# Kernel optimization log

Hardware: AMD Instinct MI355X
Metric: run time of the kernel (lower is better)

The kernel has to match this reference:

```python
import jax, jax.numpy as jnp
import numpy as np
from itertools import combinations, product

NQ = 10
DIM = 2 ** NQ
DEPTH = 1
ENC_PAIRS = [(q, q + 1) for q in range(0, NQ - 1, 2)] + [(q, q + 1) for q in range(1, NQ - 1, 2)]  # brick layer: even then odd
PYR = [(i, i + 1) for layer in range(NQ - 1) for i in range(NQ - layer - 1)]  # pyramid RBS wire pairs (45)
OBS_PAIRS = list(combinations(range(NQ), 2))  # 45 pairwise 2-local observables

_P = {'I': np.eye(2, dtype=np.complex128),
      'X': np.array([[0, 1], [1, 0]], dtype=np.complex128),
      'Y': np.array([[0, -1j], [1j, 0]], dtype=np.complex128),
      'Z': np.array([[1, 0], [0, -1]], dtype=np.complex128)}
_WORDS = [''.join(w) for w in product('IXYZ', repeat=2)][1:]  # PennyLane pauli_basis order, identity excluded
P15 = jnp.asarray(np.stack([np.kron(_P[w[0]], _P[w[1]]) for w in _WORDS]).astype(np.complex64))
XXm = jnp.asarray(np.kron(_P['X'], _P['X']).astype(np.complex64))
YYm = jnp.asarray(np.kron(_P['Y'], _P['Y']).astype(np.complex64))
ZZm = jnp.asarray(np.kron(_P['Z'], _P['Z']).astype(np.complex64))
I4 = jnp.eye(4, dtype=jnp.complex64)
_TRIL_I, _TRIL_J = np.tril_indices(4, -1)  # order matches create_Hermitian's count+j indexing


def _u3(t, p, l):
    c = jnp.cos(t / 2).astype(jnp.complex64)
    s = jnp.sin(t / 2).astype(jnp.complex64)
    return jnp.stack([jnp.stack([c, -jnp.exp(1j * l) * s]),
                      jnp.stack([jnp.exp(1j * p) * s, jnp.exp(1j * (p + l)) * c])])


def _ising(phi, P):
    # exp(-i*phi/2 * P) for P in {XX, YY, ZZ} (P^2 = I)
    return jnp.cos(phi / 2) * I4 - 1j * jnp.sin(phi / 2) * P


def _apply1(psi, U, w):
    # psi: (B, 2, ..., 2); single-qubit gate U (2,2) on wire w
    psi = jnp.moveaxis(psi, 1 + w, -1)
    sh = psi.shape
    out = jnp.einsum('ij,brj->bri', U, psi.reshape(sh[0], -1, 2)).reshape(sh)
    return jnp.moveaxis(out, -1, 1 + w)


def _apply2(psi, U, a, b):
    # two-qubit gate on wires (a,b), a is most-significant (PennyLane wire order). U: (4,4) or batched (B,4,4)
    psi = jnp.moveaxis(psi, (1 + a, 1 + b), (-2, -1))
    sh = psi.shape
    flat = psi.reshape(sh[0], -1, 4)
    eq = 'bij,brj->bri' if U.ndim == 3 else 'ij,brj->bri'
    out = jnp.einsum(eq, U, flat).reshape(sh)
    return jnp.moveaxis(out, (-2, -1), (1 + a, 1 + b))


def _build_H(A, B, D):
    # create_Hermitian: lower triangle A+iB, diag[0:3] = D[1:4], diag[3]=0, then h + h^dagger
    n = A.shape[0]
    h = jnp.zeros((n, 4, 4), jnp.complex64)
    h = h.at[:, _TRIL_I, _TRIL_J].set(A.astype(jnp.complex64) + 1j * B.astype(jnp.complex64))
    d = np.arange(3)
    h = h.at[:, d, d].set(D[:, 1:4].astype(jnp.complex64))
    return h + jnp.conj(jnp.swapaxes(h, -1, -2))


def setup_inputs() -> dict:
    key = jax.random.key(0)
    ks = jax.random.split(key, 9)
    f32 = jnp.float32
    return {
        'x': jax.random.normal(ks[0], (256, 512), f32),
        'W1': jax.random.normal(ks[1], (512, 256), f32) * (512 ** -0.5),
        'b1': jnp.zeros((256,), f32),
        'W2': jax.random.normal(ks[2], (256, 135), f32) * (256 ** -0.5),
        'b2': jnp.zeros((135,), f32),
        'qvit_params': 0.01 * jax.random.normal(ks[3], (DEPTH, len(PYR), 12), f32),
        'A': 2.0 * jax.random.normal(ks[4], (len(OBS_PAIRS), 6), f32),
        'B': 2.0 * jax.random.normal(ks[5], (len(OBS_PAIRS), 6), f32),
        'D': 2.0 * jax.random.normal(ks[6], (len(OBS_PAIRS), 4), f32),
    }


def reference(x, W1, b1, W2, b2, qvit_params, A, B, D):
    Bsz = x.shape[0]
    # enc_proj: Linear -> SiLU -> Linear
    enc = jax.nn.silu(x @ W1 + b1) @ W2 + b2  # (B, 135)
    # Brick-layer SpecialUnitary encoding: U = exp(i * sum theta_m P_m) via eigh
    theta = enc.reshape(Bsz, len(ENC_PAIRS), 15).astype(jnp.complex64)
    Hg = jnp.einsum('bgm,mij->bgij', theta, P15)  # Hermitian generators (B, 9, 4, 4)
    ew, V = jnp.linalg.eigh(Hg)
    Ue = jnp.einsum('bgik,bgk,bgjk->bgij', V, jnp.exp(1j * ew.astype(jnp.complex64)), jnp.conj(V))
    # |0...0>
    psi = jnp.zeros((Bsz, DIM), jnp.complex64).at[:, 0].set(1.0).reshape((Bsz,) + (2,) * NQ)
    for g, (a, b) in enumerate(ENC_PAIRS):
        psi = _apply2(psi, Ue[:, g], a, b)
    # QViT pyramid ansatz
    for ly in range(DEPTH):
        for g, (a, b) in enumerate(PYR):
            p = qvit_params[ly, g]
            psi = _apply1(psi, _u3(p[0], p[1], p[2]), a)
            psi = _apply2(psi, _ising(p[3], XXm), a, b)
            psi = _apply2(psi, _ising(p[4], YYm), a, b)
            psi = _apply2(psi, _ising(p[5], ZZm), a, b)
            psi = _apply1(psi, _u3(p[6], p[7], p[8]), a)
            psi = _apply2(psi, _ising(p[9], XXm), a, b)
            psi = _apply2(psi, _ising(p[10], YYm), a, b)
            psi = _apply2(psi, _ising(p[11], ZZm), a, b)
    # Pairwise ANO Hermitian expectations
    Hobs = _build_H(A, B, D)  # (45, 4, 4)
    outs = []
    for w, (a, b) in enumerate(OBS_PAIRS):
        pm = jnp.moveaxis(psi, (1 + a, 1 + b), (1, 2)).reshape(Bsz, 4, -1)
        outs.append(jnp.real(jnp.einsum('bir,ij,bjr->b', jnp.conj(pm), Hobs[w], pm)))
    return jnp.stack(outs, axis=1).astype(jnp.float32)
```

## Files before the change

kernel.cpp:

```cpp
#include <hip/hip_runtime.h>
#include <math.h>

#define NOBS 45
typedef float2 c32;

constexpr int OAc[NOBS] = {
    0,0,0,0,0,0,0,0,0, 1,1,1,1,1,1,1,1, 2,2,2,2,2,2,2, 3,3,3,3,3,3,
    4,4,4,4,4, 5,5,5,5, 6,6,6, 7,7, 8};
constexpr int OBc[NOBS] = {
    1,2,3,4,5,6,7,8,9, 2,3,4,5,6,7,8,9, 3,4,5,6,7,8,9, 4,5,6,7,8,9,
    5,6,7,8,9, 6,7,8,9, 7,8,9, 8,9, 9};

__device__ __forceinline__ c32 cfma(c32 a, c32 b, c32 c) {
    c.x = fmaf(a.x, b.x, fmaf(-a.y, b.y, c.x));
    c.y = fmaf(a.x, b.y, fmaf(a.y, b.x, c.y));
    return c;
}
__device__ __forceinline__ c32 cmul(c32 a, c32 b) {
    return make_float2(a.x * b.x - a.y * b.y, a.x * b.y + a.y * b.x);
}

template <int CTRL>
__device__ __forceinline__ float dppf(float x) {
    return __uint_as_float((unsigned)__builtin_amdgcn_update_dpp(
        0, (int)__float_as_uint(x), CTRL, 0xF, 0xF, true));
}
__device__ __forceinline__ float swap32f(float a) {
    auto r = __builtin_amdgcn_permlane32_swap(__float_as_uint(a), __float_as_uint(a), false, false);
    return (__uint_as_float(r[0]) + __uint_as_float(r[1])) - a;
}
#if __has_builtin(__builtin_amdgcn_permlane16_swap)
__device__ __forceinline__ float swap16f(float a) {
    auto r = __builtin_amdgcn_permlane16_swap(__float_as_uint(a), __float_as_uint(a), false, false);
    return (__uint_as_float(r[0]) + __uint_as_float(r[1])) - a;
}
#else
__device__ __forceinline__ float swap16f(float a) { return __shfl_xor(a, 16, 64); }
#endif
__device__ __forceinline__ float swz4f(float a) {
    return __uint_as_float(__builtin_amdgcn_ds_swizzle(__float_as_uint(a), 0x101F));
}
template <int M>
__device__ __forceinline__ float exf(float x) {
    float r = x;
    if constexpr ((M & 3) == 1) r = dppf<0xB1>(r);
    else if constexpr ((M & 3) == 2) r = dppf<0x4E>(r);
    else if constexpr ((M & 3) == 3) r = dppf<0x1B>(r);
    if constexpr (M & 4)  r = swz4f(r);
    if constexpr (M & 8)  r = dppf<0x128>(r);
    if constexpr (M & 16) r = swap16f(r);
    if constexpr (M & 32) r = swap32f(r);
    return r;
}
template <int M>
__device__ __forceinline__ c32 exch(c32 a) { return make_float2(exf<M>(a.x), exf<M>(a.y)); }

__device__ __forceinline__ float wave_reduce63(float x) {
    x += dppf<0x111>(x);
    x += dppf<0x112>(x);
    x += dppf<0x114>(x);
    x += dppf<0x118>(x);
    x += dppf<0x142>(x);
    x += dppf<0x143>(x);
    return x;
}

__device__ __forceinline__ int insert2(int t, int pl, int ph) {
    int low  = t & ((1 << pl) - 1);
    int rest = t >> pl;
    int nm   = ph - 1 - pl;
    int mid  = rest & ((1 << nm) - 1);
    int high = rest >> nm;
    return low | (mid << (pl + 1)) | (high << (ph + 1));
}

template <int W>
__device__ __forceinline__ c32 pE(int r, int c) {
    if constexpr (W == 0) return make_float2((r == c) ? 1.f : 0.f, 0.f);
    else if constexpr (W == 1) return make_float2((r != c) ? 1.f : 0.f, 0.f);
    else if constexpr (W == 2) return make_float2(0.f, (r == c) ? 0.f : ((r == 0) ? -1.f : 1.f));
    else return make_float2((r == c) ? ((r == 0) ? 1.f : -1.f) : 0.f, 0.f);
}
template <int W0, int W1>
__device__ __forceinline__ void paccum(c32& H, float th, int i1, int i2, int j1, int j2) {
    c32 a = pE<W0>(i1, j1), b = pE<W1>(i2, j2);
    c32 p = cmul(a, b);
    H.x = fmaf(th, p.x, H.x);
    H.y = fmaf(th, p.y, H.y);
}

struct F8v { c32 u[8]; };
struct FLoc { c32 a[4]; c32 b[4]; };
struct F4 { c32 uS, uB, uA, uC; };

__device__ __forceinline__ F8v loadF8(const c32* __restrict__ U, int rr) {
    F8v f;
    const c32* R = U + (rr << 3);
#pragma unroll
    for (int i = 0; i < 8; i++) f.u[i] = R[i];
    return f;
}
template <int LB>
__device__ __forceinline__ FLoc loadLocLane(const c32* __restrict__ U, int ln) {
    int lb = (ln >> LB) & 1;
    const c32* R0 = U + lb * 4;
    const c32* R1 = U + (2 | lb) * 4;
    FLoc f;
    f.a[0] = R0[lb]; f.a[1] = R0[lb ^ 1]; f.a[2] = R0[2 | lb]; f.a[3] = R0[2 | (lb ^ 1)];
    f.b[0] = R1[lb]; f.b[1] = R1[lb ^ 1]; f.b[2] = R1[2 | lb]; f.b[3] = R1[2 | (lb ^ 1)];
    return f;
}
template <int LB>
__device__ __forceinline__ void applyLocLane(c32 v[2], const FLoc& f) {
    c32 p0 = exch<(1 << LB)>(v[0]);
    c32 p1 = exch<(1 << LB)>(v[1]);
    c32 n0 = cfma(f.a[3], p1, cfma(f.a[2], v[1], cfma(f.a[1], p0, cmul(f.a[0], v[0]))));
    c32 n1 = cfma(f.b[3], p1, cfma(f.b[2], v[1], cfma(f.b[1], p0, cmul(f.b[0], v[0]))));
    v[0] = n0; v[1] = n1;
}
template <int QA, int QB>
__device__ __forceinline__ F4 loadL2(const c32* __restrict__ U, int ln) {
    int bA = (ln >> QA) & 1, bB = (ln >> QB) & 1;
    int r = (bA << 1) | bB;
    const c32* Ur = U + r * 4;
    F4 f;
    f.uS = Ur[r]; f.uB = Ur[r ^ 1]; f.uA = Ur[r ^ 2]; f.uC = Ur[r ^ 3];
    return f;
}
template <int QA, int QB>
__device__ __forceinline__ void applyL2(c32 v[2], const F4& f) {
    c32 pB[2], pA[2], pC[2];
#pragma unroll
    for (int lc = 0; lc < 2; lc++) pB[lc] = exch<(1 << QB)>(v[lc]);
#pragma unroll
    for (int lc = 0; lc < 2; lc++) pA[lc] = exch<(1 << QA)>(v[lc]);
#pragma unroll
    for (int lc = 0; lc < 2; lc++) pC[lc] = exch<(1 << QA)>(pB[lc]);
#pragma unroll
    for (int lc = 0; lc < 2; lc++)
        v[lc] = cfma(f.uC, pC[lc], cfma(f.uA, pA[lc], cfma(f.uB, pB[lc], cmul(f.uS, v[lc]))));
}

__device__ __forceinline__ void dumpV2(const c32 v[2], c32* __restrict__ psi, int t) {
    psi[t * 2] = v[0]; psi[t * 2 + 1] = v[1];
}
__device__ __forceinline__ void loadV2(c32 v[2], const c32* __restrict__ psi, int t) {
    v[0] = psi[t * 2]; v[1] = psi[t * 2 + 1];
}
template <int PA, int PB>
__device__ __forceinline__ void ldsApply2(const F8v& f, const c32* __restrict__ src,
                                          c32* __restrict__ dst, int g, int rr) {
    int base = insert2(g, PA, PB);
    constexpr int oa = 1 << PA, ob = 1 << PB;
    c32 g0 = src[base], g1 = src[base + ob], g2 = src[base + oa], g3 = src[base + oa + ob];
    c32 n0 = cfma(f.u[3], g3, cfma(f.u[2], g2, cfma(f.u[1], g1, cmul(f.u[0], g0))));
    c32 n1 = cfma(f.u[7], g3, cfma(f.u[6], g2, cfma(f.u[5], g1, cmul(f.u[4], g0))));
    dst[base + rr * oa] = n0;
    dst[base + rr * oa + ob] = n1;
}

__global__ __launch_bounds__(512, 1) void mega_kernel(
    const float* __restrict__ x,  const float* __restrict__ W1, const float* __restrict__ b1,
    const float* __restrict__ W2, const float* __restrict__ b2, const float* __restrict__ qp,
    const float* __restrict__ Am, const float* __restrict__ Bm, const float* __restrict__ Dm,
    float* __restrict__ out) {
    __shared__ __align__(16) c32 psiS[2048];
    __shared__ c32 UeS[144];
    __shared__ c32 GpS[720];
    __shared__ float HbS[720];
    __shared__ float encS0[136], encS1[136];
    __shared__ float redS[NOBS * 8];

    const int b = blockIdx.x, t = threadIdx.x, ln = t & 63;
    const int gg = t & 255, rr = t >> 8, wv = t >> 6;
    float* F = (float*)psiS;
    c32* psiA = psiS;
    c32* psiB = psiS + 1024;

    if (t < 128) ((float4*)F)[t] = ((const float4*)(x + (size_t)b * 512))[t];
    __syncthreads();
    {
        int q = t & 63, sl = t >> 6;
        float4 a4 = make_float4(0.f, 0.f, 0.f, 0.f);
#pragma unroll 16
        for (int kk = 0; kk < 64; kk++) {
            int k = sl * 64 + kk;
            float xk = F[k];
            const float4 w = *(const float4*)(W1 + (size_t)k * 256 + q * 4);
            a4.x = fmaf(xk, w.x, a4.x); a4.y = fmaf(xk, w.y, a4.y);
            a4.z = fmaf(xk, w.z, a4.z); a4.w = fmaf(xk, w.w, a4.w);
        }
        *(float4*)(F + 512 + sl * 256 + q * 4) = a4;
    }
    __syncthreads();
    if (t < 256) {
        float hv = b1[t];
#pragma unroll
        for (int s = 0; s < 8; s++) hv += F[512 + s * 256 + t];
        hv = hv / (1.f + __expf(-hv));
        F[2560 + t] = hv;
    }
    __syncthreads();
    if (t < 135) {
        float a0 = b2[t], a1 = 0.f;
#pragma unroll 16
        for (int k = 0; k < 64; k++) {
            a0 = fmaf(F[2560 + k],      W2[(size_t)k * 135 + t],        a0);
            a1 = fmaf(F[2560 + 64 + k], W2[(size_t)(64 + k) * 135 + t], a1);
        }
        encS0[t] = a0 + a1;
    } else if (t >= 256 && t < 391) {
        int c = t - 256;
        float a0 = 0.f, a1 = 0.f;
#pragma unroll 16
        for (int k = 0; k < 64; k++) {
            a0 = fmaf(F[2560 + 128 + k], W2[(size_t)(128 + k) * 135 + c], a0);
            a1 = fmaf(F[2560 + 192 + k], W2[(size_t)(192 + k) * 135 + c], a1);
        }
        encS1[c] = a0 + a1;
    }
    __syncthreads();

    c32* Mm = psiS;
    c32* Rb = psiS + 144;
    c32* TA = psiS + 288;
    if (t < 144) {
        int m = t >> 4, e = t & 15, i = e >> 2, j = e & 3;
        int i1 = i >> 1, i2 = i & 1, j1 = j >> 1, j2 = j & 1;
        const int o = m * 15;
        c32 H = make_float2(0.f, 0.f);
#define TH(J) (encS0[o + (J)] + encS1[o + (J)])
        paccum<0,1>(H, TH(0),  i1,i2,j1,j2); paccum<0,2>(H, TH(1),  i1,i2,j1,j2);
        paccum<0,3>(H, TH(2),  i1,i2,j1,j2); paccum<1,0>(H, TH(3),  i1,i2,j1,j2);
        paccum<1,1>(H, TH(4),  i1,i2,j1,j2); paccum<1,2>(H, TH(5),  i1,i2,j1,j2);
        paccum<1,3>(H, TH(6),  i1,i2,j1,j2); paccum<2,0>(H, TH(7),  i1,i2,j1,j2);
        paccum<2,1>(H, TH(8),  i1,i2,j1,j2); paccum<2,2>(H, TH(9),  i1,i2,j1,j2);
        paccum<2,3>(H, TH(10), i1,i2,j1,j2); paccum<3,0>(H, TH(11), i1,i2,j1,j2);
        paccum<3,1>(H, TH(12), i1,i2,j1,j2); paccum<3,2>(H, TH(13), i1,i2,j1,j2);
        paccum<3,3>(H, TH(14), i1,i2,j1,j2);
#undef TH
        const float sc = 1.f / 64.f;
        Mm[t] = make_float2(-H.y * sc, H.x * sc);
        Rb[t] = make_float2((i == j) ? 1.f : 0.f, 0.f);
    } else if (t >= 384 && t < 384 + NOBS) {
        const int w = t - 384;
        float* Hf = HbS + w * 16;
        Hf[0] = 2.f * Dm[w * 4 + 1];
        Hf[1] = 2.f * Dm[w * 4 + 2];
        Hf[2] = 2.f * Dm[w * 4 + 3];
        Hf[3] = 0.f;
#pragma unroll
        for (int k = 0; k < 6; k++) {
            Hf[4 + 2 * k] = 2.f * Am[w * 6 + k];
            Hf[5 + 2 * k] = 2.f * Bm[w * 6 + k];
        }
    }
    __syncthreads();
    c32 Mrow[4];
    if (t < 144) {
        int m = t >> 4, i = (t & 15) >> 2;
#pragma unroll
        for (int k = 0; k < 4; k++) Mrow[k] = Mm[m * 16 + i * 4 + k];
    }
#pragma unroll 1
    for (int step = 0; step < 13; step++) {
        if (t < 144) {
            int m = t >> 4, e = t & 15, i = e >> 2, j = e & 3;
            const c32* cur = (step & 1) ? UeS : Rb;
            c32 acc = make_float2(0.f, 0.f);
            c32 outv;
            if (step < 7) {
#pragma unroll
                for (int k = 0; k < 4; k++) acc = cfma(Mrow[k], cur[m * 16 + k * 4 + j], acc);
                float inv = 1.f / (float)(7 - step);
                outv = make_float2(fmaf(acc.x, inv, (i == j) ? 1.f : 0.f), acc.y * inv);
            } else {
#pragma unroll
                for (int k = 0; k < 4; k++)
                    acc = cfma(cur[m * 16 + i * 4 + k], cur[m * 16 + k * 4 + j], acc);
                outv = acc;
            }
            ((step & 1) ? Rb : UeS)[t] = outv;
        } else if (t >= 144 && t < 234 && step < 8) {
            int pt = t - 144, g = pt >> 1, ih = (pt & 1) << 1;
            const float* p = qp + g * 12;
            const c32* src = ((step & 1) ? TA : GpS) + g * 16;
            c32* dst = ((step & 1) ? GpS : TA) + g * 16;
#pragma unroll
            for (int r2 = 0; r2 < 2; r2++) {
                int i = ih + r2, i1 = i >> 1, i2 = i & 1;
                c32 rowv[4];
                if (step == 0) {
                    float s, c; __sincosf(p[0] * 0.5f, &s, &c);
                    c32 u0, u1;
                    if (i1 == 0) { u0 = make_float2(c, 0.f);
                                   u1 = make_float2(-__cosf(p[2]) * s, -__sinf(p[2]) * s); }
                    else { u0 = make_float2(__cosf(p[1]) * s, __sinf(p[1]) * s);
                           u1 = make_float2(__cosf(p[1] + p[2]) * c, __sinf(p[1] + p[2]) * c); }
#pragma unroll
                    for (int jj = 0; jj < 4; jj++) rowv[jj] = make_float2(0.f, 0.f);
                    rowv[i2] = u0; rowv[2 | i2] = u1;
                } else {
                    c32 coef0, coef1; int c0, c1;
                    if (step == 1 || step == 5) {
                        float s, c; __sincosf(p[step == 1 ? 3 : 9] * 0.5f, &s, &c);
                        c0 = i; coef0 = make_float2(c, 0.f);
                        c1 = i ^ 3; coef1 = make_float2(0.f, -s);
                    } else if (step == 2 || step == 6) {
                        float s, c; __sincosf(p[step == 2 ? 4 : 10] * 0.5f, &s, &c);
                        float yy = (i == 0 || i == 3) ? 1.f : -1.f;
                        c0 = i; coef0 = make_float2(c, 0.f);
                        c1 = i ^ 3; coef1 = make_float2(0.f, s * yy);
                    } else if (step == 3 || step == 7) {
                        float s, c; __sincosf(p[step == 3 ? 5 : 11] * 0.5f, &s, &c);
                        float zz = (i == 0 || i == 3) ? 1.f : -1.f;
                        c0 = i; coef0 = make_float2(c, -s * zz);
                        c1 = i; coef1 = make_float2(0.f, 0.f);
                    } else {
                        float s, c; __sincosf(p[6] * 0.5f, &s, &c);
                        if (i1 == 0) { coef0 = make_float2(c, 0.f);
                                       coef1 = make_float2(-__cosf(p[8]) * s, -__sinf(p[8]) * s); }
                        else { coef0 = make_float2(__cosf(p[7]) * s, __sinf(p[7]) * s);
                               coef1 = make_float2(__cosf(p[7] + p[8]) * c, __sinf(p[7] + p[8]) * c); }
                        c0 = i2; c1 = 2 | i2;
                    }
#pragma unroll
                    for (int jj = 0; jj < 4; jj++)
                        rowv[jj] = cfma(coef0, src[c0 * 4 + jj], cmul(coef1, src[c1 * 4 + jj]));
                }
#pragma unroll
                for (int jj = 0; jj < 4; jj++) dst[i * 4 + jj] = rowv[jj];
            }
        }
        __syncthreads();
    }

    c32 v[2];
    v[0] = make_float2(0.f, 0.f);
    v[1] = make_float2(0.f, 0.f);
    if (t == 0) v[0] = make_float2(1.f, 0.f);

    applyLocLane<0>(v, loadLocLane<0>(UeS + 0, ln));
    applyL2<1, 2>(v, loadL2<1, 2>(UeS + 16, ln));
    applyL2<3, 4>(v, loadL2<3, 4>(UeS + 32, ln));
    applyL2<0, 1>(v, loadL2<0, 1>(UeS + 80, ln));
    applyL2<2, 3>(v, loadL2<2, 3>(UeS + 96, ln));
    dumpV2(v, psiA, t); __syncthreads();
    ldsApply2<6, 7>(loadF8(UeS + 48, rr), psiA, psiB, gg, rr); __syncthreads();
    ldsApply2<8, 9>(loadF8(UeS + 64, rr), psiB, psiA, gg, rr); __syncthreads();
    loadV2(v, psiA, t);
    applyL2<4, 5>(v, loadL2<4, 5>(UeS + 112, ln));
    dumpV2(v, psiA, t); __syncthreads();
    ldsApply2<7, 8>(loadF8(UeS + 128, rr), psiA, psiB, gg, rr); __syncthreads();
    loadV2(v, psiB, t);

    {
        int g = 0;
#pragma unroll
        for (int layer = 0; layer < 9; layer++) {
            const int amax = 8 - layer;
            applyLocLane<0>(v, loadLocLane<0>(GpS + (g++) * 16, ln));
            if (amax >= 1) applyL2<0, 1>(v, loadL2<0, 1>(GpS + (g++) * 16, ln));
            if (amax >= 2) applyL2<1, 2>(v, loadL2<1, 2>(GpS + (g++) * 16, ln));
            if (amax >= 3) applyL2<2, 3>(v, loadL2<2, 3>(GpS + (g++) * 16, ln));
            if (amax >= 4) applyL2<3, 4>(v, loadL2<3, 4>(GpS + (g++) * 16, ln));
            if (amax >= 5) applyL2<4, 5>(v, loadL2<4, 5>(GpS + (g++) * 16, ln));
            if (amax >= 6) {
                dumpV2(v, psiA, t); __syncthreads();
                ldsApply2<6, 7>(loadF8(GpS + (g++) * 16, rr), psiA, psiB, gg, rr);
                __syncthreads();
                if (amax >= 7) {
                    ldsApply2<7, 8>(loadF8(GpS + (g++) * 16, rr), psiB, psiA, gg, rr);
                    __syncthreads();
                    if (amax >= 8) {
                        ldsApply2<8, 9>(loadF8(GpS + (g++) * 16, rr), psiA, psiB, gg, rr);
                        __syncthreads();
                        loadV2(v, psiB, t);
                    } else {
                        loadV2(v, psiA, t);
                    }
                } else {
                    loadV2(v, psiB, t);
                }
            }
        }
    }

    dumpV2(v, psiA, t);
    __syncthreads();
#pragma unroll
    for (int w0 = 0; w0 < NOBS; w0 += 5) {
        float pr[5];
#pragma unroll
        for (int u = 0; u < 5; u++) {
            const int w = w0 + u;
            const int pa = OAc[w], pb = OBc[w];
            const int oa = 1 << pa, ob = 1 << pb;
            int i0 = insert2(gg, pa, pb);
            const float* Hf = HbS + w * 16;
            c32 g0 = psiA[i0], g1 = psiA[i0 + ob], g2 = psiA[i0 + oa], g3 = psiA[i0 + oa + ob];
            float r;
            if (rr == 0) {
                r = Hf[0] * fmaf(g0.x, g0.x, g0.y * g0.y)
                  + Hf[1] * fmaf(g1.x, g1.x, g1.y * g1.y)
                  + Hf[2] * fmaf(g2.x, g2.x, g2.y * g2.y);
                float cx0 = fmaf(g1.x, g0.x, g1.y * g0.y);
                float cy0 = fmaf(g1.x, g0.y, -g1.y * g0.x);
                r = fmaf(Hf[4], cx0, r); r = fmaf(-Hf[5], cy0, r);
                float cx1 = fmaf(g2.x, g0.x, g2.y * g0.y);
                float cy1 = fmaf(g2.x, g0.y, -g2.y * g0.x);
                r = fmaf(Hf[6], cx1, r); r = fmaf(-Hf[7], cy1, r);
            } else {
                float cx0 = fmaf(g2.x, g1.x, g2.y * g1.y);
                float cy0 = fmaf(g2.x, g1.y, -g2.y * g1.x);
                r = Hf[8] * cx0 - Hf[9] * cy0;
                float cx1 = fmaf(g3.x, g0.x, g3.y * g0.y);
                float cy1 = fmaf(g3.x, g0.y, -g3.y * g0.x);
                r = fmaf(Hf[10], cx1, r); r = fmaf(-Hf[11], cy1, r);
                float cx2 = fmaf(g3.x, g1.x, g3.y * g1.y);
                float cy2 = fmaf(g3.x, g1.y, -g3.y * g1.x);
                r = fmaf(Hf[12], cx2, r); r = fmaf(-Hf[13], cy2, r);
                float cx3 = fmaf(g3.x, g2.x, g3.y * g2.y);
                float cy3 = fmaf(g3.x, g2.y, -g3.y * g2.x);
                r = fmaf(Hf[14], cx3, r); r = fmaf(-Hf[15], cy3, r);
            }
            pr[u] = wave_reduce63(r);
        }
        if (ln == 63) {
#pragma unroll
            for (int u = 0; u < 5; u++) redS[(w0 + u) * 8 + wv] = pr[u];
        }
    }
    __syncthreads();
    if (t < NOBS) {
        float s = 0.f;
#pragma unroll
        for (int k = 0; k < 8; k++) s += redS[t * 8 + k];
        out[(size_t)b * NOBS + t] = s;
    }
}

extern "C" void kernel_launch(void* const* d_in, const int* in_sizes, int n_in,
                              void* d_out, int out_size, void* d_ws, size_t ws_size,
                              hipStream_t stream) {
    (void)in_sizes; (void)n_in; (void)out_size; (void)d_ws; (void)ws_size;
    const float* x  = (const float*)d_in[0];
    const float* W1 = (const float*)d_in[1];
    const float* b1 = (const float*)d_in[2];
    const float* W2 = (const float*)d_in[3];
    const float* b2 = (const float*)d_in[4];
    const float* qp = (const float*)d_in[5];
    const float* Am = (const float*)d_in[6];
    const float* Bm = (const float*)d_in[7];
    const float* Dm = (const float*)d_in[8];
    float* out = (float*)d_out;

    hipLaunchKernelGGL(mega_kernel, dim3(256), dim3(512), 0, stream,
                       x, W1, b1, W2, b2, qp, Am, Bm, Dm, out);
}
```

Before: 105.6 us.

## Remap wire-to-slot layout and batch gate coefficient loads ahead of apply

Introduces a wire-to-storage-bit permutation that moves wire 3 to a high slot and wires 4-6 down, so more gates act on register/lane-local bits and the LDS-based two-qubit steps use different bit pairs. Gate coefficient loads for each pyramid layer and for the encoder are hoisted before a scheduling barrier, and the observable phase batches LDS amplitude reads before the arithmetic. This is meant to hide LDS load latency and reduce expensive cross-lane or LDS gate passes, at the cost of higher register pressure and a more intricate index mapping.

```diff
diff --git a/kernel.cpp b/kernel.cpp
--- a/kernel.cpp
+++ b/kernel.cpp
@@ -4,12 +4,15 @@
 #define NOBS 45
 typedef float2 c32;
 
+constexpr int W2S[10] = {0, 1, 2, 4, 5, 6, 3, 7, 8, 9};
 constexpr int OAc[NOBS] = {
     0,0,0,0,0,0,0,0,0, 1,1,1,1,1,1,1,1, 2,2,2,2,2,2,2, 3,3,3,3,3,3,
     4,4,4,4,4, 5,5,5,5, 6,6,6, 7,7, 8};
 constexpr int OBc[NOBS] = {
     1,2,3,4,5,6,7,8,9, 2,3,4,5,6,7,8,9, 3,4,5,6,7,8,9, 4,5,6,7,8,9,
     5,6,7,8,9, 6,7,8,9, 7,8,9, 8,9, 9};
+
+#define SCHED_FENCE() __builtin_amdgcn_sched_barrier(0)
 
 __device__ __forceinline__ c32 cfma(c32 a, c32 b, c32 c) {
     c.x = fmaf(a.x, b.x, fmaf(-a.y, b.y, c.x));
@@ -340,41 +343,64 @@
     v[1] = make_float2(0.f, 0.f);
     if (t == 0) v[0] = make_float2(1.f, 0.f);
 
-    applyLocLane<0>(v, loadLocLane<0>(UeS + 0, ln));
-    applyL2<1, 2>(v, loadL2<1, 2>(UeS + 16, ln));
-    applyL2<3, 4>(v, loadL2<3, 4>(UeS + 32, ln));
-    applyL2<0, 1>(v, loadL2<0, 1>(UeS + 80, ln));
-    applyL2<2, 3>(v, loadL2<2, 3>(UeS + 96, ln));
-    dumpV2(v, psiA, t); __syncthreads();
-    ldsApply2<6, 7>(loadF8(UeS + 48, rr), psiA, psiB, gg, rr); __syncthreads();
-    ldsApply2<8, 9>(loadF8(UeS + 64, rr), psiB, psiA, gg, rr); __syncthreads();
-    loadV2(v, psiA, t);
-    applyL2<4, 5>(v, loadL2<4, 5>(UeS + 112, ln));
-    dumpV2(v, psiA, t); __syncthreads();
-    ldsApply2<7, 8>(loadF8(UeS + 128, rr), psiA, psiB, gg, rr); __syncthreads();
-    loadV2(v, psiB, t);
+    {
+        FLoc e0 = loadLocLane<0>(UeS + 0, ln);
+        F4 e1 = loadL2<1, 3>(UeS + 16, ln);
+        F4 e2 = loadL2<4, 5>(UeS + 32, ln);
+        F4 e3 = loadL2<0, 1>(UeS + 80, ln);
+        F4 e4 = loadL2<3, 4>(UeS + 96, ln);
+        F8v e5 = loadF8(UeS + 48, rr);
+        F8v e6 = loadF8(UeS + 64, rr);
+        SCHED_FENCE();
+        applyLocLane<0>(v, e0);
+        applyL2<1, 3>(v, e1);
+        applyL2<4, 5>(v, e2);
+        applyL2<0, 1>(v, e3);
+        applyL2<3, 4>(v, e4);
+        dumpV2(v, psiA, t); __syncthreads();
+        ldsApply2<3, 7>(e5, psiA, psiB, gg, rr); __syncthreads();
+        ldsApply2<8, 9>(e6, psiB, psiA, gg, rr); __syncthreads();
+        loadV2(v, psiA, t);
+        F4 e7 = loadL2<5, 2>(UeS + 112, ln);
+        F8v e8 = loadF8(UeS + 128, rr);
+        SCHED_FENCE();
+        applyL2<5, 2>(v, e7);
+        dumpV2(v, psiA, t); __syncthreads();
+        ldsApply2<7, 8>(e8, psiA, psiB, gg, rr); __syncthreads();
+        loadV2(v, psiB, t);
+    }
 
     {
         int g = 0;
 #pragma unroll
         for (int layer = 0; layer < 9; layer++) {
             const int amax = 8 - layer;
-            applyLocLane<0>(v, loadLocLane<0>(GpS + (g++) * 16, ln));
-            if (amax >= 1) applyL2<0, 1>(v, loadL2<0, 1>(GpS + (g++) * 16, ln));
-            if (amax >= 2) applyL2<1, 2>(v, loadL2<1, 2>(GpS + (g++) * 16, ln));
-            if (amax >= 3) applyL2<2, 3>(v, loadL2<2, 3>(GpS + (g++) * 16, ln));
-            if (amax >= 4) applyL2<3, 4>(v, loadL2<3, 4>(GpS + (g++) * 16, ln));
-            if (amax >= 5) applyL2<4, 5>(v, loadL2<4, 5>(GpS + (g++) * 16, ln));
+            FLoc h0 = loadLocLane<0>(GpS + g * 16, ln);
+            F4 h1, h2, h3, h4, h5;
+            F8v q1, q2, q3;
+            int gi = g + 1;
+            if (amax >= 1) h1 = loadL2<0, 1>(GpS + (gi++) * 16, ln);
+            if (amax >= 2) h2 = loadL2<1, 3>(GpS + (gi++) * 16, ln);
+            if (amax >= 3) h3 = loadL2<3, 4>(GpS + (gi++) * 16, ln);
+            if (amax >= 4) h4 = loadL2<4, 5>(GpS + (gi++) * 16, ln);
+            if (amax >= 5) h5 = loadL2<5, 2>(GpS + (gi++) * 16, ln);
+            if (amax >= 6) q1 = loadF8(GpS + (gi++) * 16, rr);
+            if (amax >= 7) q2 = loadF8(GpS + (gi++) * 16, rr);
+            if (amax >= 8) q3 = loadF8(GpS + (gi++) * 16, rr);
+            SCHED_FENCE();
+            applyLocLane<0>(v, h0);
+            if (amax >= 1) applyL2<0, 1>(v, h1);
+            if (amax >= 2) applyL2<1, 3>(v, h2);
+            if (amax >= 3) applyL2<3, 4>(v, h3);
+            if (amax >= 4) applyL2<4, 5>(v, h4);
+            if (amax >= 5) applyL2<5, 2>(v, h5);
             if (amax >= 6) {
                 dumpV2(v, psiA, t); __syncthreads();
-                ldsApply2<6, 7>(loadF8(GpS + (g++) * 16, rr), psiA, psiB, gg, rr);
-                __syncthreads();
+                ldsApply2<3, 7>(q1, psiA, psiB, gg, rr); __syncthreads();
                 if (amax >= 7) {
-                    ldsApply2<7, 8>(loadF8(GpS + (g++) * 16, rr), psiB, psiA, gg, rr);
-                    __syncthreads();
+                    ldsApply2<7, 8>(q2, psiB, psiA, gg, rr); __syncthreads();
                     if (amax >= 8) {
-                        ldsApply2<8, 9>(loadF8(GpS + (g++) * 16, rr), psiA, psiB, gg, rr);
-                        __syncthreads();
+                        ldsApply2<8, 9>(q3, psiA, psiB, gg, rr); __syncthreads();
                         loadV2(v, psiB, t);
                     } else {
                         loadV2(v, psiA, t);
@@ -383,6 +409,7 @@
                     loadV2(v, psiB, t);
                 }
             }
+            g = gi;
         }
     }
 
@@ -390,15 +417,24 @@
     __syncthreads();
 #pragma unroll
     for (int w0 = 0; w0 < NOBS; w0 += 5) {
-        float pr[5];
+        c32 vg[5][4];
 #pragma unroll
         for (int u = 0; u < 5; u++) {
             const int w = w0 + u;
-            const int pa = OAc[w], pb = OBc[w];
+            const int pa = W2S[OAc[w]], pb = W2S[OBc[w]];
+            const int pl = (pa < pb) ? pa : pb, ph = (pa < pb) ? pb : pa;
             const int oa = 1 << pa, ob = 1 << pb;
-            int i0 = insert2(gg, pa, pb);
+            int i0 = insert2(gg, pl, ph);
+            vg[u][0] = psiA[i0];      vg[u][1] = psiA[i0 + ob];
+            vg[u][2] = psiA[i0 + oa]; vg[u][3] = psiA[i0 + oa + ob];
+        }
+        SCHED_FENCE();
+        float pr[5];
+#pragma unroll
+        for (int u = 0; u < 5; u++) {
+            const int w = w0 + u;
             const float* Hf = HbS + w * 16;
-            c32 g0 = psiA[i0], g1 = psiA[i0 + ob], g2 = psiA[i0 + oa], g3 = psiA[i0 + oa + ob];
+            c32 g0 = vg[u][0], g1 = vg[u][1], g2 = vg[u][2], g3 = vg[u][3];
             float r;
             if (rr == 0) {
                 r = Hf[0] * fmaf(g0.x, g0.x, g0.y * g0.y)
```

After: 107.6 us. About the same (+2.0%).

## Use 1024 threads with one amplitude per thread and remap qubits to lanes

Applied to the files above, without the earlier changes.

Doubles the block to 1024 threads so each thread holds a single state amplitude instead of two. Qubits are permuted so more gates act on lane bits through cross-lane exchanges, and the rest use LDS passes with one output per thread. Gate coefficients are loaded up front behind a scheduling barrier so LDS reads can overlap. The MLP and observable stages are split across the larger thread count. The cost is more threads per block and possibly higher register pressure under the new launch bounds.

```diff
diff --git a/kernel.cpp b/kernel.cpp
--- a/kernel.cpp
+++ b/kernel.cpp
@@ -4,12 +4,15 @@
 #define NOBS 45
 typedef float2 c32;
 
+constexpr int W2S[10] = {0, 1, 3, 4, 5, 2, 6, 7, 8, 9};
 constexpr int OAc[NOBS] = {
     0,0,0,0,0,0,0,0,0, 1,1,1,1,1,1,1,1, 2,2,2,2,2,2,2, 3,3,3,3,3,3,
     4,4,4,4,4, 5,5,5,5, 6,6,6, 7,7, 8};
 constexpr int OBc[NOBS] = {
     1,2,3,4,5,6,7,8,9, 2,3,4,5,6,7,8,9, 3,4,5,6,7,8,9, 4,5,6,7,8,9,
     5,6,7,8,9, 6,7,8,9, 7,8,9, 8,9, 9};
+
+#define SCHED_FENCE() __builtin_amdgcn_sched_barrier(0)
 
 __device__ __forceinline__ c32 cfma(c32 a, c32 b, c32 c) {
     c.x = fmaf(a.x, b.x, fmaf(-a.y, b.y, c.x));
@@ -89,35 +92,9 @@
     H.y = fmaf(th, p.y, H.y);
 }
 
-struct F8v { c32 u[8]; };
-struct FLoc { c32 a[4]; c32 b[4]; };
 struct F4 { c32 uS, uB, uA, uC; };
-
-__device__ __forceinline__ F8v loadF8(const c32* __restrict__ U, int rr) {
-    F8v f;
-    const c32* R = U + (rr << 3);
-#pragma unroll
-    for (int i = 0; i < 8; i++) f.u[i] = R[i];
-    return f;
-}
-template <int LB>
-__device__ __forceinline__ FLoc loadLocLane(const c32* __restrict__ U, int ln) {
-    int lb = (ln >> LB) & 1;
-    const c32* R0 = U + lb * 4;
-    const c32* R1 = U + (2 | lb) * 4;
-    FLoc f;
-    f.a[0] = R0[lb]; f.a[1] = R0[lb ^ 1]; f.a[2] = R0[2 | lb]; f.a[3] = R0[2 | (lb ^ 1)];
-    f.b[0] = R1[lb]; f.b[1] = R1[lb ^ 1]; f.b[2] = R1[2 | lb]; f.b[3] = R1[2 | (lb ^ 1)];
-    return f;
-}
-template <int LB>
-__device__ __forceinline__ void applyLocLane(c32 v[2], const FLoc& f) {
-    c32 p0 = exch<(1 << LB)>(v[0]);
-    c32 p1 = exch<(1 << LB)>(v[1]);
-    c32 n0 = cfma(f.a[3], p1, cfma(f.a[2], v[1], cfma(f.a[1], p0, cmul(f.a[0], v[0]))));
-    c32 n1 = cfma(f.b[3], p1, cfma(f.b[2], v[1], cfma(f.b[1], p0, cmul(f.b[0], v[0]))));
-    v[0] = n0; v[1] = n1;
-}
+struct F4row { c32 u[4]; };
+
 template <int QA, int QB>
 __device__ __forceinline__ F4 loadL2(const c32* __restrict__ U, int ln) {
     int bA = (ln >> QA) & 1, bB = (ln >> QB) & 1;
@@ -128,38 +105,32 @@
     return f;
 }
 template <int QA, int QB>
-__device__ __forceinline__ void applyL2(c32 v[2], const F4& f) {
-    c32 pB[2], pA[2], pC[2];
-#pragma unroll
-    for (int lc = 0; lc < 2; lc++) pB[lc] = exch<(1 << QB)>(v[lc]);
-#pragma unroll
-    for (int lc = 0; lc < 2; lc++) pA[lc] = exch<(1 << QA)>(v[lc]);
-#pragma unroll
-    for (int lc = 0; lc < 2; lc++) pC[lc] = exch<(1 << QA)>(pB[lc]);
-#pragma unroll
-    for (int lc = 0; lc < 2; lc++)
-        v[lc] = cfma(f.uC, pC[lc], cfma(f.uA, pA[lc], cfma(f.uB, pB[lc], cmul(f.uS, v[lc]))));
-}
-
-__device__ __forceinline__ void dumpV2(const c32 v[2], c32* __restrict__ psi, int t) {
-    psi[t * 2] = v[0]; psi[t * 2 + 1] = v[1];
-}
-__device__ __forceinline__ void loadV2(c32 v[2], const c32* __restrict__ psi, int t) {
-    v[0] = psi[t * 2]; v[1] = psi[t * 2 + 1];
+__device__ __forceinline__ void applyL2(c32& v, const F4& f) {
+    c32 pB = exch<(1 << QB)>(v);
+    c32 pA = exch<(1 << QA)>(v);
+    c32 pC = exch<(1 << QA)>(pB);
+    v = cfma(f.uC, pC, cfma(f.uA, pA, cfma(f.uB, pB, cmul(f.uS, v))));
+}
+
+__device__ __forceinline__ F4row loadF4row(const c32* __restrict__ U, int rr) {
+    F4row f;
+    const c32* R = U + (rr << 2);
+#pragma unroll
+    for (int i = 0; i < 4; i++) f.u[i] = R[i];
+    return f;
 }
 template <int PA, int PB>
-__device__ __forceinline__ void ldsApply2(const F8v& f, const c32* __restrict__ src,
+__device__ __forceinline__ void ldsApply1(const F4row& f, const c32* __restrict__ src,
                                           c32* __restrict__ dst, int g, int rr) {
-    int base = insert2(g, PA, PB);
+    constexpr int PL = (PA < PB) ? PA : PB, PH = (PA < PB) ? PB : PA;
+    int base = insert2(g, PL, PH);
     constexpr int oa = 1 << PA, ob = 1 << PB;
     c32 g0 = src[base], g1 = src[base + ob], g2 = src[base + oa], g3 = src[base + oa + ob];
-    c32 n0 = cfma(f.u[3], g3, cfma(f.u[2], g2, cfma(f.u[1], g1, cmul(f.u[0], g0))));
-    c32 n1 = cfma(f.u[7], g3, cfma(f.u[6], g2, cfma(f.u[5], g1, cmul(f.u[4], g0))));
-    dst[base + rr * oa] = n0;
-    dst[base + rr * oa + ob] = n1;
-}
-
-__global__ __launch_bounds__(512, 1) void mega_kernel(
+    c32 n = cfma(f.u[3], g3, cfma(f.u[2], g2, cfma(f.u[1], g1, cmul(f.u[0], g0))));
+    dst[base + (rr >> 1) * oa + (rr & 1) * ob] = n;
+}
+
+__global__ __launch_bounds__(1024, 4) void mega_kernel(
     const float* __restrict__ x,  const float* __restrict__ W1, const float* __restrict__ b1,
     const float* __restrict__ W2, const float* __restrict__ b2, const float* __restrict__ qp,
     const float* __restrict__ Am, const float* __restrict__ Bm, const float* __restrict__ Dm,
@@ -168,56 +139,48 @@
     __shared__ c32 UeS[144];
     __shared__ c32 GpS[720];
     __shared__ float HbS[720];
-    __shared__ float encS0[136], encS1[136];
-    __shared__ float redS[NOBS * 8];
+    __shared__ float encS[4][136];
+    __shared__ float redS[NOBS * 16];
 
     const int b = blockIdx.x, t = threadIdx.x, ln = t & 63;
-    const int gg = t & 255, rr = t >> 8, wv = t >> 6;
+    const int g4 = t >> 2, rr4 = t & 3, wv = t >> 6;
     float* F = (float*)psiS;
     c32* psiA = psiS;
     c32* psiB = psiS + 1024;
 
-    if (t < 128) ((float4*)F)[t] = ((const float4*)(x + (size_t)b * 512))[t];
-    __syncthreads();
     {
-        int q = t & 63, sl = t >> 6;
+        const int q = t & 63, sl = t >> 6;
+        const float* xrow = x + (size_t)b * 512 + sl * 32;
         float4 a4 = make_float4(0.f, 0.f, 0.f, 0.f);
-#pragma unroll 16
-        for (int kk = 0; kk < 64; kk++) {
-            int k = sl * 64 + kk;
-            float xk = F[k];
-            const float4 w = *(const float4*)(W1 + (size_t)k * 256 + q * 4);
+#pragma unroll 8
+        for (int kk = 0; kk < 32; kk++) {
+            float xk = xrow[kk];
+            const float4 w = *(const float4*)(W1 + (size_t)(sl * 32 + kk) * 256 + q * 4);
             a4.x = fmaf(xk, w.x, a4.x); a4.y = fmaf(xk, w.y, a4.y);
             a4.z = fmaf(xk, w.z, a4.z); a4.w = fmaf(xk, w.w, a4.w);
         }
-        *(float4*)(F + 512 + sl * 256 + q * 4) = a4;
+        *(float4*)(F + sl * 256 + q * 4) = a4;
     }
     __syncthreads();
     if (t < 256) {
         float hv = b1[t];
 #pragma unroll
-        for (int s = 0; s < 8; s++) hv += F[512 + s * 256 + t];
+        for (int s = 0; s < 16; s++) hv += F[s * 256 + t];
         hv = hv / (1.f + __expf(-hv));
-        F[2560 + t] = hv;
-    }
-    __syncthreads();
-    if (t < 135) {
-        float a0 = b2[t], a1 = 0.f;
+        F[t] = hv;
+    }
+    __syncthreads();
+    {
+        int ks = t >> 8, col = t & 255;
+        if (col < 135) {
+            float a = (ks == 0) ? b2[col] : 0.f;
 #pragma unroll 16
-        for (int k = 0; k < 64; k++) {
-            a0 = fmaf(F[2560 + k],      W2[(size_t)k * 135 + t],        a0);
-            a1 = fmaf(F[2560 + 64 + k], W2[(size_t)(64 + k) * 135 + t], a1);
-        }
-        encS0[t] = a0 + a1;
-    } else if (t >= 256 && t < 391) {
-        int c = t - 256;
-        float a0 = 0.f, a1 = 0.f;
-#pragma unroll 16
-        for (int k = 0; k < 64; k++) {
-            a0 = fmaf(F[2560 + 128 + k], W2[(size_t)(128 + k) * 135 + c], a0);
-            a1 = fmaf(F[2560 + 192 + k], W2[(size_t)(192 + k) * 135 + c], a1);
-        }
-        encS1[c] = a0 + a1;
+            for (int kk = 0; kk < 64; kk++) {
+                int k = ks * 64 + kk;
+                a = fmaf(F[k], W2[(size_t)k * 135 + col], a);
+            }
+            encS[ks][col] = a;
+        }
     }
     __syncthreads();
 
@@ -229,7 +192,7 @@
         int i1 = i >> 1, i2 = i & 1, j1 = j >> 1, j2 = j & 1;
         const int o = m * 15;
         c32 H = make_float2(0.f, 0.f);
-#define TH(J) (encS0[o + (J)] + encS1[o + (J)])
+#define TH(J) (encS[0][o + (J)] + encS[1][o + (J)] + encS[2][o + (J)] + encS[3][o + (J)])
         paccum<0,1>(H, TH(0),  i1,i2,j1,j2); paccum<0,2>(H, TH(1),  i1,i2,j1,j2);
         paccum<0,3>(H, TH(2),  i1,i2,j1,j2); paccum<1,0>(H, TH(3),  i1,i2,j1,j2);
         paccum<1,1>(H, TH(4),  i1,i2,j1,j2); paccum<1,2>(H, TH(5),  i1,i2,j1,j2);
@@ -335,58 +298,80 @@
         __syncthreads();
     }
 
-    c32 v[2];
-    v[0] = make_float2(0.f, 0.f);
-    v[1] = make_float2(0.f, 0.f);
-    if (t == 0) v[0] = make_float2(1.f, 0.f);
-
-    applyLocLane<0>(v, loadLocLane<0>(UeS + 0, ln));
-    applyL2<1, 2>(v, loadL2<1, 2>(UeS + 16, ln));
-    applyL2<3, 4>(v, loadL2<3, 4>(UeS + 32, ln));
-    applyL2<0, 1>(v, loadL2<0, 1>(UeS + 80, ln));
-    applyL2<2, 3>(v, loadL2<2, 3>(UeS + 96, ln));
-    dumpV2(v, psiA, t); __syncthreads();
-    ldsApply2<6, 7>(loadF8(UeS + 48, rr), psiA, psiB, gg, rr); __syncthreads();
-    ldsApply2<8, 9>(loadF8(UeS + 64, rr), psiB, psiA, gg, rr); __syncthreads();
-    loadV2(v, psiA, t);
-    applyL2<4, 5>(v, loadL2<4, 5>(UeS + 112, ln));
-    dumpV2(v, psiA, t); __syncthreads();
-    ldsApply2<7, 8>(loadF8(UeS + 128, rr), psiA, psiB, gg, rr); __syncthreads();
-    loadV2(v, psiB, t);
+    c32 v = (t == 0) ? make_float2(1.f, 0.f) : make_float2(0.f, 0.f);
+
+    {
+        F4 e0 = loadL2<0, 1>(UeS + 0, ln);
+        F4 e1 = loadL2<3, 4>(UeS + 16, ln);
+        F4 e2 = loadL2<5, 2>(UeS + 32, ln);
+        F4 e3 = loadL2<1, 3>(UeS + 80, ln);
+        F4 e4 = loadL2<4, 5>(UeS + 96, ln);
+        F4row q67 = loadF4row(UeS + 48, rr4);
+        F4row q89 = loadF4row(UeS + 64, rr4);
+        F4row q56 = loadF4row(UeS + 112, rr4);
+        F4row q78 = loadF4row(UeS + 128, rr4);
+        SCHED_FENCE();
+        applyL2<0, 1>(v, e0);
+        applyL2<3, 4>(v, e1);
+        applyL2<5, 2>(v, e2);
+        applyL2<1, 3>(v, e3);
+        applyL2<4, 5>(v, e4);
+        psiA[t] = v; __syncthreads();
+        ldsApply1<6, 7>(q67, psiA, psiB, g4, rr4); __syncthreads();
+        ldsApply1<8, 9>(q89, psiB, psiA, g4, rr4); __syncthreads();
+        ldsApply1<2, 6>(q56, psiA, psiB, g4, rr4); __syncthreads();
+        ldsApply1<7, 8>(q78, psiB, psiA, g4, rr4); __syncthreads();
+        v = psiA[t];
+    }
 
     {
         int g = 0;
 #pragma unroll
         for (int layer = 0; layer < 9; layer++) {
             const int amax = 8 - layer;
-            applyLocLane<0>(v, loadLocLane<0>(GpS + (g++) * 16, ln));
-            if (amax >= 1) applyL2<0, 1>(v, loadL2<0, 1>(GpS + (g++) * 16, ln));
-            if (amax >= 2) applyL2<1, 2>(v, loadL2<1, 2>(GpS + (g++) * 16, ln));
-            if (amax >= 3) applyL2<2, 3>(v, loadL2<2, 3>(GpS + (g++) * 16, ln));
-            if (amax >= 4) applyL2<3, 4>(v, loadL2<3, 4>(GpS + (g++) * 16, ln));
-            if (amax >= 5) applyL2<4, 5>(v, loadL2<4, 5>(GpS + (g++) * 16, ln));
-            if (amax >= 6) {
-                dumpV2(v, psiA, t); __syncthreads();
-                ldsApply2<6, 7>(loadF8(GpS + (g++) * 16, rr), psiA, psiB, gg, rr);
-                __syncthreads();
-                if (amax >= 7) {
-                    ldsApply2<7, 8>(loadF8(GpS + (g++) * 16, rr), psiB, psiA, gg, rr);
-                    __syncthreads();
-                    if (amax >= 8) {
-                        ldsApply2<8, 9>(loadF8(GpS + (g++) * 16, rr), psiA, psiB, gg, rr);
-                        __syncthreads();
-                        loadV2(v, psiB, t);
+            F4 h0 = loadL2<0, 1>(GpS + g * 16, ln);
+            F4 h1, h2, h3, h4;
+            F4row q5, q6, q7, q8;
+            int gi = g + 1;
+            if (amax >= 1) h1 = loadL2<1, 3>(GpS + (gi++) * 16, ln);
+            if (amax >= 2) h2 = loadL2<3, 4>(GpS + (gi++) * 16, ln);
+            if (amax >= 3) h3 = loadL2<4, 5>(GpS + (gi++) * 16, ln);
+            if (amax >= 4) h4 = loadL2<5, 2>(GpS + (gi++) * 16, ln);
+            if (amax >= 5) q5 = loadF4row(GpS + (gi++) * 16, rr4);
+            if (amax >= 6) q6 = loadF4row(GpS + (gi++) * 16, rr4);
+            if (amax >= 7) q7 = loadF4row(GpS + (gi++) * 16, rr4);
+            if (amax >= 8) q8 = loadF4row(GpS + (gi++) * 16, rr4);
+            SCHED_FENCE();
+            applyL2<0, 1>(v, h0);
+            if (amax >= 1) applyL2<1, 3>(v, h1);
+            if (amax >= 2) applyL2<3, 4>(v, h2);
+            if (amax >= 3) applyL2<4, 5>(v, h3);
+            if (amax >= 4) applyL2<5, 2>(v, h4);
+            if (amax >= 5) {
+                psiA[t] = v; __syncthreads();
+                ldsApply1<2, 6>(q5, psiA, psiB, g4, rr4); __syncthreads();
+                if (amax >= 6) {
+                    ldsApply1<6, 7>(q6, psiB, psiA, g4, rr4); __syncthreads();
+                    if (amax >= 7) {
+                        ldsApply1<7, 8>(q7, psiA, psiB, g4, rr4); __syncthreads();
+                        if (amax >= 8) {
+                            ldsApply1<8, 9>(q8, psiB, psiA, g4, rr4); __syncthreads();
+                            v = psiA[t];
+                        } else {
+                            v = psiB[t];
+                        }
                     } else {
-                        loadV2(v, psiA, t);
+                        v = psiA[t];
                     }
                 } else {
-                    loadV2(v, psiB, t);
+                    v = psiB[t];
                 }
             }
-        }
-    }
-
-    dumpV2(v, psiA, t);
+            g = gi;
+        }
+    }
+
+    psiA[t] = v;
     __syncthreads();
 #pragma unroll
     for (int w0 = 0; w0 < NOBS; w0 += 5) {
@@ -394,48 +379,51 @@
 #pragma unroll
         for (int u = 0; u < 5; u++) {
             const int w = w0 + u;
-            const int pa = OAc[w], pb = OBc[w];
+            const int pa = W2S[OAc[w]], pb = W2S[OBc[w]];
+            const int pl = (pa < pb) ? pa : pb, ph = (pa < pb) ? pb : pa;
             const int oa = 1 << pa, ob = 1 << pb;
-            int i0 = insert2(gg, pa, pb);
+            int i0 = insert2(g4, pl, ph);
+            c32 g0 = psiA[i0], g1 = psiA[i0 + ob], g2 = psiA[i0 + oa], g3 = psiA[i0 + oa + ob];
             const float* Hf = HbS + w * 16;
-            c32 g0 = psiA[i0], g1 = psiA[i0 + ob], g2 = psiA[i0 + oa], g3 = psiA[i0 + oa + ob];
             float r;
-            if (rr == 0) {
+            if (rr4 == 0) {
                 r = Hf[0] * fmaf(g0.x, g0.x, g0.y * g0.y)
-                  + Hf[1] * fmaf(g1.x, g1.x, g1.y * g1.y)
-                  + Hf[2] * fmaf(g2.x, g2.x, g2.y * g2.y);
-                float cx0 = fmaf(g1.x, g0.x, g1.y * g0.y);
-                float cy0 = fmaf(g1.x, g0.y, -g1.y * g0.x);
-                r = fmaf(Hf[4], cx0, r); r = fmaf(-Hf[5], cy0, r);
-                float cx1 = fmaf(g2.x, g0.x, g2.y * g0.y);
-                float cy1 = fmaf(g2.x, g0.y, -g2.y * g0.x);
-                r = fmaf(Hf[6], cx1, r); r = fmaf(-Hf[7], cy1, r);
+                  + Hf[1] * fmaf(g1.x, g1.x, g1.y * g1.y);
+            } else if (rr4 == 1) {
+                r = Hf[2] * fmaf(g2.x, g2.x, g2.y * g2.y);
+                float cx = fmaf(g1.x, g0.x, g1.y * g0.y);
+                float cy = fmaf(g1.x, g0.y, -g1.y * g0.x);
+                r = fmaf(Hf[4], cx, r); r = fmaf(-Hf[5], cy, r);
+            } else if (rr4 == 2) {
+                float cx0 = fmaf(g2.x, g0.x, g2.y * g0.y);
+                float cy0 = fmaf(g2.x, g0.y, -g2.y * g0.x);
+                r = Hf[6] * cx0 - Hf[7] * cy0;
+                float cx1 = fmaf(g2.x, g1.x, g2.y * g1.y);
+                float cy1 = fmaf(g2.x, g1.y, -g2.y * g1.x);
+                r = fmaf(Hf[8], cx1, r); r = fmaf(-Hf[9], cy1, r);
             } else {
-                float cx0 = fmaf(g2.x, g1.x, g2.y * g1.y);
-                float cy0 = fmaf(g2.x, g1.y, -g2.y * g1.x);
-                r = Hf[8] * cx0 - Hf[9] * cy0;
-                float cx1 = fmaf(g3.x, g0.x, g3.y * g0.y);
-                float cy1 = fmaf(g3.x, g0.y, -g3.y * g0.x);
-                r = fmaf(Hf[10], cx1, r); r = fmaf(-Hf[11], cy1, r);
-                float cx2 = fmaf(g3.x, g1.x, g3.y * g1.y);
-                float cy2 = fmaf(g3.x, g1.y, -g3.y * g1.x);
-                r = fmaf(Hf[12], cx2, r); r = fmaf(-Hf[13], cy2, r);
-                float cx3 = fmaf(g3.x, g2.x, g3.y * g2.y);
-                float cy3 = fmaf(g3.x, g2.y, -g3.y * g2.x);
-                r = fmaf(Hf[14], cx3, r); r = fmaf(-Hf[15], cy3, r);
+                float cx0 = fmaf(g3.x, g0.x, g3.y * g0.y);
+                float cy0 = fmaf(g3.x, g0.y, -g3.y * g0.x);
+                r = Hf[10] * cx0 - Hf[11] * cy0;
+                float cx1 = fmaf(g3.x, g1.x, g3.y * g1.y);
+                float cy1 = fmaf(g3.x, g1.y, -g3.y * g1.x);
+                r = fmaf(Hf[12], cx1, r); r = fmaf(-Hf[13], cy1, r);
+                float cx2 = fmaf(g3.x, g2.x, g3.y * g2.y);
+                float cy2 = fmaf(g3.x, g2.y, -g3.y * g2.x);
+                r = fmaf(Hf[14], cx2, r); r = fmaf(-Hf[15], cy2, r);
             }
             pr[u] = wave_reduce63(r);
         }
         if (ln == 63) {
 #pragma unroll
-            for (int u = 0; u < 5; u++) redS[(w0 + u) * 8 + wv] = pr[u];
+            for (int u = 0; u < 5; u++) redS[(w0 + u) * 16 + wv] = pr[u];
         }
     }
     __syncthreads();
     if (t < NOBS) {
         float s = 0.f;
 #pragma unroll
-        for (int k = 0; k < 8; k++) s += redS[t * 8 + k];
+        for (int k = 0; k < 16; k++) s += redS[t * 16 + k];
         out[(size_t)b * NOBS + t] = s;
     }
 }
@@ -455,6 +443,6 @@
     const float* Dm = (const float*)d_in[8];
     float* out = (float*)d_out;
 
-    hipLaunchKernelGGL(mega_kernel, dim3(256), dim3(512), 0, stream,
+    hipLaunchKernelGGL(mega_kernel, dim3(256), dim3(1024), 0, stream,
                        x, W1, b1, W2, b2, qp, Am, Bm, Dm, out);
 }
```

Result: slower. 119.3 us (+13.0%).
